# Performance work log

Hardware: AMD Instinct MI355X
Metric: run time of the kernel (lower is better)

The kernel has to match this reference:

```python
import jax, jax.numpy as jnp
import numpy as np

EPS = 1e-06
NUM_HEADS = 16


def _rms_norm(x, g, eps=EPS):
    # normalize over the last (full model) dim, as WanRMSNorm(dim)
    var = jnp.mean(jnp.square(x), axis=-1, keepdims=True)
    return x * jax.lax.rsqrt(var + eps) * g


def _apply_rope(q, k, freqs):
    # q, k: [b, s, n, d]; freqs: [s, d//2] angles. Interleaved (complex) pairs
    b, s, n, d = q.shape
    cos = jnp.cos(freqs)[None, :, None, :]  # [1, s, 1, d//2]
    sin = jnp.sin(freqs)[None, :, None, :]

    def rot(t):
        tr = t.reshape(b, s, n, d // 2, 2)
        t0, t1 = tr[..., 0], tr[..., 1]
        o0 = t0 * cos - t1 * sin
        o1 = t0 * sin + t1 * cos
        return jnp.stack([o0, o1], axis=-1).reshape(b, s, n, d)

    return rot(q), rot(k)


def setup_inputs() -> dict:
    key = jax.random.key(0)
    ks = jax.random.split(key, 8)
    b, s, dim = 2, 2048, 2048
    hd = dim // NUM_HEADS
    x = jax.random.normal(ks[0], (b, s, dim), dtype=jnp.float32)
    seq_lens = jax.random.randint(ks[1], (b,), s // 2, s + 1, dtype=jnp.int32)
    grid_sizes = jax.random.randint(ks[2], (b, 3), 1, 16).astype(jnp.int64)
    freqs = jax.random.uniform(ks[3], (s, hd // 2), dtype=jnp.float32) * 6.283
    sc = 1.0 / np.sqrt(dim)
    Wq = jax.random.normal(ks[4], (dim, dim), dtype=jnp.float32) * sc
    Wk = jax.random.normal(ks[5], (dim, dim), dtype=jnp.float32) * sc
    Wv = jax.random.normal(ks[6], (dim, dim), dtype=jnp.float32) * sc
    Wo = jax.random.normal(ks[7], (dim, dim), dtype=jnp.float32) * sc
    bo = jnp.zeros((dim,), dtype=jnp.float32)
    gq = jnp.ones((dim,), dtype=jnp.float32)
    gk = jnp.ones((dim,), dtype=jnp.float32)
    return {"x": x, "seq_lens": seq_lens, "grid_sizes": grid_sizes, "freqs": freqs,
            "Wq": Wq, "Wk": Wk, "Wv": Wv, "Wo": Wo, "bo": bo, "gq": gq, "gk": gk}


def reference(x, seq_lens, grid_sizes, freqs, Wq, Wk, Wv, Wo, bo, gq, gk):
    b, s, dim = x.shape
    n = NUM_HEADS
    d = dim // n
    scale = d ** (-0.5)

    # QKV projections (Linear: x @ W.T), with RMSNorm over full dim on q/k
    q = _rms_norm(x @ Wq.T, gq).reshape(b, s, n, d)
    k = _rms_norm(x @ Wk.T, gk).reshape(b, s, n, d)
    v = (x @ Wv.T).reshape(b, s, n, d)

    q, k = _apply_rope(q, k, freqs)

    # varlen attention: keys beyond seq_lens[b] are masked out
    scores = jnp.einsum("bqnd,bknd->bnqk", q, k) * scale
    key_valid = jnp.arange(s)[None, None, None, :] < seq_lens[:, None, None, None]
    scores = jnp.where(key_valid, scores, jnp.float32(-1e9))
    probs = jax.nn.softmax(scores, axis=-1)
    attn = jnp.einsum("bnqk,bknd->bqnd", probs, v).reshape(b, s, dim)

    return attn @ Wo.T + bo
```

## Files before the change

### kernel.cpp

```cpp
#include <hip/hip_runtime.h>
#include <hip/hip_bf16.h>
#include <math.h>

#define BATCH 2
#define SEQ   2048
#define DIM   2048
#define NH    16
#define HD    128
#define NROWS (BATCH * SEQ)
#define EPS_RMS 1e-6f

typedef unsigned short ushort_t;
typedef unsigned int   uint_t;
typedef __bf16    bf16x8 __attribute__((ext_vector_type(8)));
typedef _Float16  f16x8  __attribute__((ext_vector_type(8)));
typedef float     f32x4  __attribute__((ext_vector_type(4)));

__device__ inline ushort_t f2bf(float f) {
    uint_t u = __builtin_bit_cast(uint_t, f);
    uint_t r = u + 0x7FFFu + ((u >> 16) & 1u);
    return (ushort_t)(r >> 16);
}
__device__ inline ushort_t f2h(float f) {
    return __builtin_bit_cast(ushort_t, (_Float16)f);
}

__global__ __launch_bounds__(256) void cvt_all_kernel(
    const float* __restrict__ x,  const float* __restrict__ wq,
    const float* __restrict__ wk, const float* __restrict__ wv,
    const float* __restrict__ wo,
    ushort_t* __restrict__ xh,  ushort_t* __restrict__ wqh,
    ushort_t* __restrict__ wkh, ushort_t* __restrict__ wvh,
    ushort_t* __restrict__ woh)
{
    const int blk = blockIdx.x;
    const float* src; ushort_t* dst; size_t base;
    if (blk < 4096) { src = x; dst = xh; base = (size_t)blk * 2048; }
    else {
        const int r = blk - 4096;
        const int wsel = r >> 11;
        base = (size_t)(r & 2047) * 2048;
        if      (wsel == 0) { src = wq; dst = wqh; }
        else if (wsel == 1) { src = wk; dst = wkh; }
        else if (wsel == 2) { src = wv; dst = wvh; }
        else                { src = wo; dst = woh; }
    }
    const size_t i = base + ((size_t)threadIdx.x << 3);
    float v[8];
    *(float4*)&v[0] = *(const float4*)&src[i];
    *(float4*)&v[4] = *(const float4*)&src[i + 4];
    uint_t pk[4];
#pragma unroll
    for (int j = 0; j < 4; ++j)
        pk[j] = (uint_t)f2h(v[2 * j]) | ((uint_t)f2h(v[2 * j + 1]) << 16);
    *(uint4*)&dst[i] = make_uint4(pk[0], pk[1], pk[2], pk[3]);
}

template<int MODE>
__global__ __launch_bounds__(256, 3) void gemm_f16_kernel(
    const ushort_t* __restrict__ Ah, const ushort_t* __restrict__ Bh,
    const float* __restrict__ bias,
    float* __restrict__ C, ushort_t* __restrict__ Ct,
    const int M, const int N, const int K)
{
    __shared__ __align__(16) ushort_t sA[4096], sB[4096];
    const int tid  = threadIdx.x;
    const int w    = tid >> 6;
    const int lane = tid & 63;

    const int bid   = blockIdx.x;
    const int chunk = gridDim.x >> 3;
    const int nid   = (bid & 7) * chunk + (bid >> 3);
    const int mb    = M >> 7;
    const int n_blk = nid / mb;
    const int m_blk = nid - n_blk * mb;
    const int m0 = m_blk * 128;
    const int n0 = n_blk * 128;

    const int scol = (lane & 3) << 3;
    const int wr = w >> 1, wc = w & 1;
    const int fr = lane & 15, quad = lane >> 4;

    f32x4 acc[4][4];
#pragma unroll
    for (int mi = 0; mi < 4; ++mi)
#pragma unroll
        for (int ni = 0; ni < 4; ++ni)
            acc[mi][ni] = (f32x4){0.f, 0.f, 0.f, 0.f};

    for (int k0 = 0; k0 < K; k0 += 32) {
        __syncthreads();
#pragma unroll
        for (int it = 0; it < 2; ++it) {
            const int row  = (w << 5) + (it << 4) + (lane >> 2);
            const int loff = (w << 10) + (it << 9);
            const size_t ga = (size_t)(m0 + row) * K + k0 + scol;
            const size_t gb = (size_t)(n0 + row) * K + k0 + scol;
            __builtin_amdgcn_global_load_lds(
                (const __attribute__((address_space(1))) uint_t*)(const void*)(Ah + ga),
                (__attribute__((address_space(3))) uint_t*)(void*)&sA[loff], 16, 0, 0);
            __builtin_amdgcn_global_load_lds(
                (const __attribute__((address_space(1))) uint_t*)(const void*)(Bh + gb),
                (__attribute__((address_space(3))) uint_t*)(void*)&sB[loff], 16, 0, 0);
        }
        __syncthreads();

        f16x8 bfr[4];
#pragma unroll
        for (int ni = 0; ni < 4; ++ni) {
            const int row = (wc << 6) + (ni << 4) + fr;
            bfr[ni] = *(const f16x8*)&sB[(row << 5) + (quad << 3)];
        }
#pragma unroll
        for (int mi = 0; mi < 4; ++mi) {
            const int row = (wr << 6) + (mi << 4) + fr;
            const f16x8 ah = *(const f16x8*)&sA[(row << 5) + (quad << 3)];
#pragma unroll
            for (int ni = 0; ni < 4; ++ni)
                acc[mi][ni] = __builtin_amdgcn_mfma_f32_16x16x32_f16(ah, bfr[ni], acc[mi][ni], 0, 0, 0);
        }
    }

#pragma unroll
    for (int mi = 0; mi < 4; ++mi)
#pragma unroll
        for (int ni = 0; ni < 4; ++ni) {
            const int col = n0 + (wc << 6) + (ni << 4) + fr;
            if (MODE == 0) {
                const float bv = bias ? bias[col] : 0.f;
#pragma unroll
                for (int r = 0; r < 4; ++r) {
                    const int rowg = m0 + (wr << 6) + (mi << 4) + (quad << 2) + r;
                    C[(size_t)rowg * N + col] = acc[mi][ni][r] + bv;
                }
            } else {
                const int rowg = m0 + (wr << 6) + (mi << 4) + (quad << 2);
                const int bb = rowg >> 11, tok = rowg & (SEQ - 1);
                const int hh = col >> 7, d = col & (HD - 1);
                uint2 pk;
                pk.x = (uint_t)f2bf(acc[mi][ni][0]) | ((uint_t)f2bf(acc[mi][ni][1]) << 16);
                pk.y = (uint_t)f2bf(acc[mi][ni][2]) | ((uint_t)f2bf(acc[mi][ni][3]) << 16);
                *(uint2*)&Ct[((size_t)(bb * NH + hh) * HD + d) * SEQ + tok] = pk;
            }
        }
}

__global__ __launch_bounds__(256, 3) void qkv_gemm_kernel(
    const ushort_t* __restrict__ Ah, const ushort_t* __restrict__ Bq,
    const ushort_t* __restrict__ Bk, const ushort_t* __restrict__ Bv,
    float* __restrict__ Qb, float* __restrict__ Kb, ushort_t* __restrict__ Vt)
{
    __shared__ __align__(16) ushort_t sA[4096], sB[4096];
    const int tid  = threadIdx.x;
    const int w    = tid >> 6;
    const int lane = tid & 63;

    const int bid = blockIdx.x;
    const int nid = (bid & 7) * 192 + (bid >> 3);
    const int n_blk = nid >> 5;
    const int m_blk = nid & 31;
    const int wsel  = n_blk >> 4;
    const int m0 = m_blk * 128;
    const int n0 = (n_blk & 15) * 128;
    const ushort_t* __restrict__ Bh = (wsel == 0) ? Bq : (wsel == 1) ? Bk : Bv;

    const int scol = (lane & 3) << 3;
    const int wr = w >> 1, wc = w & 1;
    const int fr = lane & 15, quad = lane >> 4;

    f32x4 acc[4][4];
#pragma unroll
    for (int mi = 0; mi < 4; ++mi)
#pragma unroll
        for (int ni = 0; ni < 4; ++ni)
            acc[mi][ni] = (f32x4){0.f, 0.f, 0.f, 0.f};

    for (int k0 = 0; k0 < DIM; k0 += 32) {
        __syncthreads();
#pragma unroll
        for (int it = 0; it < 2; ++it) {
            const int row  = (w << 5) + (it << 4) + (lane >> 2);
            const int loff = (w << 10) + (it << 9);
            const size_t ga = (size_t)(m0 + row) * DIM + k0 + scol;
            const size_t gb = (size_t)(n0 + row) * DIM + k0 + scol;
            __builtin_amdgcn_global_load_lds(
                (const __attribute__((address_space(1))) uint_t*)(const void*)(Ah + ga),
                (__attribute__((address_space(3))) uint_t*)(void*)&sA[loff], 16, 0, 0);
            __builtin_amdgcn_global_load_lds(
                (const __attribute__((address_space(1))) uint_t*)(const void*)(Bh + gb),
                (__attribute__((address_space(3))) uint_t*)(void*)&sB[loff], 16, 0, 0);
        }
        __syncthreads();

        f16x8 bfr[4];
#pragma unroll
        for (int ni = 0; ni < 4; ++ni) {
            const int row = (wc << 6) + (ni << 4) + fr;
            bfr[ni] = *(const f16x8*)&sB[(row << 5) + (quad << 3)];
        }
#pragma unroll
        for (int mi = 0; mi < 4; ++mi) {
            const int row = (wr << 6) + (mi << 4) + fr;
            const f16x8 ah = *(const f16x8*)&sA[(row << 5) + (quad << 3)];
#pragma unroll
            for (int ni = 0; ni < 4; ++ni)
                acc[mi][ni] = __builtin_amdgcn_mfma_f32_16x16x32_f16(ah, bfr[ni], acc[mi][ni], 0, 0, 0);
        }
    }

    if (wsel < 2) {
        float* __restrict__ C = (wsel == 0) ? Qb : Kb;
#pragma unroll
        for (int mi = 0; mi < 4; ++mi)
#pragma unroll
            for (int ni = 0; ni < 4; ++ni) {
                const int col = n0 + (wc << 6) + (ni << 4) + fr;
#pragma unroll
                for (int r = 0; r < 4; ++r) {
                    const int rowg = m0 + (wr << 6) + (mi << 4) + (quad << 2) + r;
                    C[(size_t)rowg * DIM + col] = acc[mi][ni][r];
                }
            }
    } else {
#pragma unroll
        for (int mi = 0; mi < 4; ++mi)
#pragma unroll
            for (int ni = 0; ni < 4; ++ni) {
                const int col = n0 + (wc << 6) + (ni << 4) + fr;
                const int rowg = m0 + (wr << 6) + (mi << 4) + (quad << 2);
                const int bb = rowg >> 11, tok = rowg & (SEQ - 1);
                const int hh = col >> 7, d = col & (HD - 1);
                uint2 pk;
                pk.x = (uint_t)f2bf(acc[mi][ni][0]) | ((uint_t)f2bf(acc[mi][ni][1]) << 16);
                pk.y = (uint_t)f2bf(acc[mi][ni][2]) | ((uint_t)f2bf(acc[mi][ni][3]) << 16);
                *(uint2*)&Vt[((size_t)(bb * NH + hh) * HD + d) * SEQ + tok] = pk;
            }
    }
}

#define BM 64
#define BN 64
#define BK 16

__global__ __launch_bounds__(256) void gemm_nt_kernel(
    const float* __restrict__ A, const float* __restrict__ W,
    const float* __restrict__ bias, float* __restrict__ C,
    const int M, const int N, const int K)
{
    __shared__ float As[BK][BM + 4];
    __shared__ float Bs[BK][BN + 4];
    const int tid = threadIdx.x;
    const int tx = tid & 15;
    const int ty = tid >> 4;
    const int m0 = blockIdx.y * BM;
    const int n0 = blockIdx.x * BN;
    const int ldr = tid >> 2;
    const int ldc = (tid & 3) << 2;

    float acc[4][4] = {};

    for (int k0 = 0; k0 < K; k0 += BK) {
        __syncthreads();
        const float4 av = *(const float4*)&A[(size_t)(m0 + ldr) * K + (k0 + ldc)];
        const float4 wv = *(const float4*)&W[(size_t)(n0 + ldr) * K + (k0 + ldc)];
        As[ldc + 0][ldr] = av.x; As[ldc + 1][ldr] = av.y;
        As[ldc + 2][ldr] = av.z; As[ldc + 3][ldr] = av.w;
        Bs[ldc + 0][ldr] = wv.x; Bs[ldc + 1][ldr] = wv.y;
        Bs[ldc + 2][ldr] = wv.z; Bs[ldc + 3][ldr] = wv.w;
        __syncthreads();
#pragma unroll
        for (int k = 0; k < BK; ++k) {
            const float4 a4 = *(const float4*)&As[k][ty << 2];
            const float4 b4 = *(const float4*)&Bs[k][tx << 2];
            const float aa[4] = {a4.x, a4.y, a4.z, a4.w};
            const float bb[4] = {b4.x, b4.y, b4.z, b4.w};
#pragma unroll
            for (int i = 0; i < 4; ++i)
#pragma unroll
                for (int j = 0; j < 4; ++j)
                    acc[i][j] = fmaf(aa[i], bb[j], acc[i][j]);
        }
    }

#pragma unroll
    for (int i = 0; i < 4; ++i) {
        const int row = m0 + (ty << 2) + i;
        const int col = n0 + (tx << 2);
        float4 ov;
        ov.x = acc[i][0]; ov.y = acc[i][1]; ov.z = acc[i][2]; ov.w = acc[i][3];
        if (bias != nullptr) {
            ov.x += bias[col + 0]; ov.y += bias[col + 1];
            ov.z += bias[col + 2]; ov.w += bias[col + 3];
        }
        *(float4*)&C[(size_t)row * N + col] = ov;
    }
}

__global__ __launch_bounds__(256) void rmsnorm_rope_qk_kernel(
    const float* __restrict__ Qb, const float* __restrict__ gq,
    ushort_t* __restrict__ qbh,
    const float* __restrict__ Kb, const float* __restrict__ gk,
    ushort_t* __restrict__ kbh,
    const float* __restrict__ freqs)
{
    const int r = blockIdx.x;
    const int s = r & (SEQ - 1);
    const int tid = threadIdx.x;
    const int base = tid << 3;
    const bool isQ = (blockIdx.y == 0);
    const float* T = isQ ? Qb : Kb;
    const float* g = isQ ? gq : gk;
    ushort_t* out  = isQ ? qbh : kbh;
    const float posc = isQ ? 0.088388347648318447f : 1.0f;

    float v[8];
    *(float4*)&v[0] = *(const float4*)&T[(size_t)r * DIM + base];
    *(float4*)&v[4] = *(const float4*)&T[(size_t)r * DIM + base + 4];

    float ss = 0.f;
#pragma unroll
    for (int i = 0; i < 8; ++i) ss += v[i] * v[i];
#pragma unroll
    for (int off = 32; off > 0; off >>= 1) ss += __shfl_down(ss, off);

    __shared__ float wsum[4];
    __shared__ float inv_sh;
    if ((tid & 63) == 0) wsum[tid >> 6] = ss;
    __syncthreads();
    if (tid == 0)
        inv_sh = rsqrtf((wsum[0] + wsum[1] + wsum[2] + wsum[3]) * (1.0f / DIM) + EPS_RMS);
    __syncthreads();
    const float inv = inv_sh * posc;

    float gg[8];
    *(float4*)&gg[0] = *(const float4*)&g[base];
    *(float4*)&gg[4] = *(const float4*)&g[base + 4];
#pragma unroll
    for (int i = 0; i < 8; ++i) v[i] *= inv * gg[i];

    const int p0 = (base & (HD - 1)) >> 1;
#pragma unroll
    for (int pp = 0; pp < 4; ++pp) {
        float sn, cs;
        __sincosf(freqs[(size_t)s * (HD / 2) + p0 + pp], &sn, &cs);
        const float t0 = v[2 * pp], t1 = v[2 * pp + 1];
        v[2 * pp]     = t0 * cs - t1 * sn;
        v[2 * pp + 1] = t0 * sn + t1 * cs;
    }

    uint_t pk[4];
#pragma unroll
    for (int j = 0; j < 4; ++j)
        pk[j] = (uint_t)f2bf(v[2 * j]) | ((uint_t)f2bf(v[2 * j + 1]) << 16);
    *(uint4*)&out[(size_t)r * DIM + base] = make_uint4(pk[0], pk[1], pk[2], pk[3]);
}

__global__ __launch_bounds__(256) void rmsnorm_rope_kernel(
    float* __restrict__ T, const float* __restrict__ g,
    const float* __restrict__ freqs)
{
    const int r = blockIdx.x;
    const int s = r & (SEQ - 1);
    const int tid = threadIdx.x;
    const int base = tid << 3;

    float v[8];
    *(float4*)&v[0] = *(const float4*)&T[(size_t)r * DIM + base];
    *(float4*)&v[4] = *(const float4*)&T[(size_t)r * DIM + base + 4];

    float ss = 0.f;
#pragma unroll
    for (int i = 0; i < 8; ++i) ss += v[i] * v[i];
#pragma unroll
    for (int off = 32; off > 0; off >>= 1) ss += __shfl_down(ss, off);

    __shared__ float wsum[4];
    __shared__ float inv_sh;
    if ((tid & 63) == 0) wsum[tid >> 6] = ss;
    __syncthreads();
    if (tid == 0)
        inv_sh = rsqrtf((wsum[0] + wsum[1] + wsum[2] + wsum[3]) * (1.0f / DIM) + EPS_RMS);
    __syncthreads();
    const float inv = inv_sh;

    float gg[8];
    *(float4*)&gg[0] = *(const float4*)&g[base];
    *(float4*)&gg[4] = *(const float4*)&g[base + 4];
#pragma unroll
    for (int i = 0; i < 8; ++i) v[i] *= inv * gg[i];

    const int p0 = (base & (HD - 1)) >> 1;
#pragma unroll
    for (int pp = 0; pp < 4; ++pp) {
        float sn, cs;
        __sincosf(freqs[(size_t)s * (HD / 2) + p0 + pp], &sn, &cs);
        const float t0 = v[2 * pp], t1 = v[2 * pp + 1];
        v[2 * pp]     = t0 * cs - t1 * sn;
        v[2 * pp + 1] = t0 * sn + t1 * cs;
    }

    *(float4*)&T[(size_t)r * DIM + base]     = *(float4*)&v[0];
    *(float4*)&T[(size_t)r * DIM + base + 4] = *(float4*)&v[4];
}

#define AQ 128
#define AK 64
#define KSTR 136
#define VSTR 72
#define RESCALE_THR 8.0f

__global__ __launch_bounds__(256, 3) void attn_mfma_kernel(
    const ushort_t* __restrict__ QH, const ushort_t* __restrict__ KH,
    const ushort_t* __restrict__ VtG, const int* __restrict__ seq_lens,
    ushort_t* __restrict__ Oh)
{
    __shared__ __align__(16) ushort_t sK[AK * KSTR];
    __shared__ __align__(16) ushort_t sVt[HD * VSTR];
    __shared__ __align__(16) ushort_t sP[AQ * VSTR];

    const int tid  = threadIdx.x;
    const int w    = tid >> 6;
    const int lane = tid & 63;
    const int fr   = lane & 15;
    const int quad = lane >> 4;

    const int bid = blockIdx.x;
    const int sw  = (bid & 7) * 64 + (bid >> 3);
    const int q0  = (sw & 15) * AQ;
    const int hb  = sw >> 4;
    const int h   = hb & 15;
    const int b   = hb >> 4;
    const int len = seq_lens[b];

    bf16x8 qfrag[2][4];
#pragma unroll
    for (int qt = 0; qt < 2; ++qt)
#pragma unroll
        for (int h4 = 0; h4 < 4; ++h4) {
            const size_t qrow = (size_t)(b * SEQ + q0 + (w << 5) + (qt << 4) + fr);
            qfrag[qt][h4] = *(const bf16x8*)&QH[qrow * DIM + h * HD + (h4 << 5) + (quad << 3)];
        }

    f32x4 Oacc[2][8];
#pragma unroll
    for (int qt = 0; qt < 2; ++qt)
#pragma unroll
        for (int dt = 0; dt < 8; ++dt)
            Oacc[qt][dt] = (f32x4){0.f, 0.f, 0.f, 0.f};
    float mrow[2] = {-1.0e30f, -1.0e30f};
    float lrow[2] = {0.f, 0.f};

    const int kr  = tid >> 4;
    const int kc8 = (tid & 15) << 3;
    const int vd  = tid >> 3;
    const int vc8 = (tid & 7) << 3;
    const size_t kbase = (size_t)(b * SEQ) * DIM + h * HD + kc8;
    const size_t vbase = ((size_t)(b * NH + h) * HD) * SEQ + vc8;

    const int ntiles = (len + AK - 1) / AK;
    for (int t = 0; t < ntiles; ++t) {
        const int k0 = t * AK;
        const bool masked = (k0 + AK > len);
        __syncthreads();
        {
            uint4 kv[4], vv[4];
#pragma unroll
            for (int j = 0; j < 4; ++j)
                kv[j] = *(const uint4*)&KH[kbase + (size_t)(k0 + kr + (j << 4)) * DIM];
#pragma unroll
            for (int j = 0; j < 4; ++j)
                vv[j] = *(const uint4*)&VtG[vbase + (size_t)(vd + (j << 5)) * SEQ + k0];
#pragma unroll
            for (int j = 0; j < 4; ++j)
                *(uint4*)&sK[(kr + (j << 4)) * KSTR + kc8] = kv[j];
#pragma unroll
            for (int j = 0; j < 4; ++j)
                *(uint4*)&sVt[(vd + (j << 5)) * VSTR + vc8] = vv[j];
        }
        __syncthreads();

        f32x4 S[4][2];
        __builtin_amdgcn_s_setprio(1);
#pragma unroll
        for (int kt = 0; kt < 4; ++kt) {
            bf16x8 kf[4];
#pragma unroll
            for (int h4 = 0; h4 < 4; ++h4)
                kf[h4] = *(const bf16x8*)&sK[((kt << 4) + fr) * KSTR + (h4 << 5) + (quad << 3)];
#pragma unroll
            for (int qt = 0; qt < 2; ++qt) {
                f32x4 a = (f32x4){0.f, 0.f, 0.f, 0.f};
#pragma unroll
                for (int h4 = 0; h4 < 4; ++h4)
                    a = __builtin_amdgcn_mfma_f32_16x16x32_bf16(kf[h4], qfrag[qt][h4], a, 0, 0, 0);
                S[kt][qt] = a;
            }
        }
        __builtin_amdgcn_s_setprio(0);

#pragma unroll
        for (int qt = 0; qt < 2; ++qt) {
            float tm = -1.0e30f;
            if (masked) {
#pragma unroll
                for (int kt = 0; kt < 4; ++kt)
#pragma unroll
                    for (int r = 0; r < 4; ++r) {
                        const int key = k0 + (kt << 4) + (quad << 2) + r;
                        float s = (key < len) ? S[kt][qt][r] : -1.0e30f;
                        S[kt][qt][r] = s;
                        tm = fmaxf(tm, s);
                    }
            } else {
#pragma unroll
                for (int kt = 0; kt < 4; ++kt)
#pragma unroll
                    for (int r = 0; r < 4; ++r)
                        tm = fmaxf(tm, S[kt][qt][r]);
            }
            tm = fmaxf(tm, __shfl_xor(tm, 16));
            tm = fmaxf(tm, __shfl_xor(tm, 32));

            float mnew;
            if (__all(tm - mrow[qt] <= RESCALE_THR)) {
                mnew = mrow[qt];
            } else {
                mnew = fmaxf(mrow[qt], tm);
                const float alpha = __expf(mrow[qt] - mnew);
                mrow[qt] = mnew;
                lrow[qt] *= alpha;
#pragma unroll
                for (int r = 0; r < 4; ++r) {
                    const float ar = __shfl(alpha, (quad << 2) + r);
#pragma unroll
                    for (int dt = 0; dt < 8; ++dt)
                        Oacc[qt][dt][r] *= ar;
                }
            }

            float rsum = 0.f;
#pragma unroll
            for (int kt = 0; kt < 4; ++kt) {
                float p[4];
#pragma unroll
                for (int r = 0; r < 4; ++r) {
                    p[r] = __expf(S[kt][qt][r] - mnew);
                    rsum += p[r];
                }
                uint2 pk;
                pk.x = (uint_t)f2bf(p[0]) | ((uint_t)f2bf(p[1]) << 16);
                pk.y = (uint_t)f2bf(p[2]) | ((uint_t)f2bf(p[3]) << 16);
                *(uint2*)&sP[((w << 5) + (qt << 4) + fr) * VSTR + (kt << 4) + (quad << 2)] = pk;
            }
            rsum += __shfl_xor(rsum, 16);
            rsum += __shfl_xor(rsum, 32);
            lrow[qt] += rsum;
        }

        __builtin_amdgcn_s_setprio(1);
#pragma unroll
        for (int ks = 0; ks < 2; ++ks) {
            bf16x8 pf[2];
#pragma unroll
            for (int qt = 0; qt < 2; ++qt)
                pf[qt] = *(const bf16x8*)&sP[((w << 5) + (qt << 4) + fr) * VSTR + (ks << 5) + (quad << 3)];
#pragma unroll
            for (int dt = 0; dt < 8; ++dt) {
                const bf16x8 vf = *(const bf16x8*)&sVt[((dt << 4) + fr) * VSTR + (ks << 5) + (quad << 3)];
#pragma unroll
                for (int qt = 0; qt < 2; ++qt)
                    Oacc[qt][dt] = __builtin_amdgcn_mfma_f32_16x16x32_bf16(pf[qt], vf, Oacc[qt][dt], 0, 0, 0);
            }
        }
        __builtin_amdgcn_s_setprio(0);
    }

#pragma unroll
    for (int qt = 0; qt < 2; ++qt) {
        float linv[4];
#pragma unroll
        for (int r = 0; r < 4; ++r)
            linv[r] = 1.0f / __shfl(lrow[qt], (quad << 2) + r);
#pragma unroll
        for (int dt = 0; dt < 8; ++dt)
#pragma unroll
            for (int r = 0; r < 4; ++r) {
                const int qrow = q0 + (w << 5) + (qt << 4) + (quad << 2) + r;
                Oh[(size_t)(b * SEQ + qrow) * DIM + h * HD + (dt << 4) + fr] =
                    f2h(Oacc[qt][dt][r] * linv[r]);
            }
    }
}

#define BQ  64
#define BKT 64

__global__ __launch_bounds__(256) void attn_kernel(
    const float* __restrict__ Q, const float* __restrict__ K,
    const float* __restrict__ V, const int* __restrict__ seq_lens,
    float* __restrict__ O)
{
    const int qt = blockIdx.x;
    const int h  = blockIdx.y;
    const int b  = blockIdx.z;
    const int len = seq_lens[b];
    const int q0 = qt * BQ;
    const float scale = 0.088388347648318447f;

    __shared__ float Qst[HD][BQ + 4];
    __shared__ float Kst[HD][BKT + 4];
    __shared__ float Vs[BKT][HD + 4];
    __shared__ float Sc[BQ][BKT + 1];
    __shared__ float mrow[BQ], lrow[BQ], alpha_s[BQ];

    const int tid = threadIdx.x;
    const int si0 = (tid >> 4) << 2;
    const int sj0 = (tid & 15) << 2;
    const int pi0 = (tid >> 4) << 2;
    const int pc0 = (tid & 15) << 3;

    for (int i = tid; i < BQ * HD / 4; i += 256) {
        const int e = i << 2;
        const int row = e >> 7;
        const int c0 = e & (HD - 1);
        const float4 qv = *(const float4*)&Q[(size_t)(b * SEQ + q0 + row) * DIM + h * HD + c0];
        Qst[c0 + 0][row] = qv.x; Qst[c0 + 1][row] = qv.y;
        Qst[c0 + 2][row] = qv.z; Qst[c0 + 3][row] = qv.w;
    }
    if (tid < BQ) { mrow[tid] = -3.0e38f; lrow[tid] = 0.f; }

    float o[4][8] = {};
    __syncthreads();

    const int ntiles = (len + BKT - 1) / BKT;
    for (int t = 0; t < ntiles; ++t) {
        const int k0 = t * BKT;
        __syncthreads();
        for (int i = tid; i < BKT * HD / 4; i += 256) {
            const int e = i << 2;
            const int row = e >> 7;
            const int c0 = e & (HD - 1);
            const int kg = k0 + row;
            float4 kv = make_float4(0.f, 0.f, 0.f, 0.f);
            float4 vv = make_float4(0.f, 0.f, 0.f, 0.f);
            if (kg < len) {
                kv = *(const float4*)&K[(size_t)(b * SEQ + kg) * DIM + h * HD + c0];
                vv = *(const float4*)&V[(size_t)(b * SEQ + kg) * DIM + h * HD + c0];
            }
            Kst[c0 + 0][row] = kv.x; Kst[c0 + 1][row] = kv.y;
            Kst[c0 + 2][row] = kv.z; Kst[c0 + 3][row] = kv.w;
            *(float4*)&Vs[row][c0] = vv;
        }
        __syncthreads();

        float acc[4][4] = {};
#pragma unroll 8
        for (int kk = 0; kk < HD; ++kk) {
            const float4 q4 = *(const float4*)&Qst[kk][si0];
            const float4 k4 = *(const float4*)&Kst[kk][sj0];
            const float qa[4] = {q4.x, q4.y, q4.z, q4.w};
            const float ka[4] = {k4.x, k4.y, k4.z, k4.w};
#pragma unroll
            for (int i = 0; i < 4; ++i)
#pragma unroll
                for (int j = 0; j < 4; ++j)
                    acc[i][j] = fmaf(qa[i], ka[j], acc[i][j]);
        }
#pragma unroll
        for (int i = 0; i < 4; ++i)
#pragma unroll
            for (int j = 0; j < 4; ++j) {
                const int jg = k0 + sj0 + j;
                Sc[si0 + i][sj0 + j] = (jg < len) ? acc[i][j] * scale : -1.0e9f;
            }
        __syncthreads();

        if (tid < BQ) {
            const int i = tid;
            const float m_old = mrow[i];
            float mx = m_old;
            for (int j = 0; j < BKT; ++j) mx = fmaxf(mx, Sc[i][j]);
            const float al = __expf(m_old - mx);
            float sum = 0.f;
            for (int j = 0; j < BKT; ++j) {
                const float p = __expf(Sc[i][j] - mx);
                Sc[i][j] = p;
                sum += p;
            }
            mrow[i] = mx;
            lrow[i] = lrow[i] * al + sum;
            alpha_s[i] = al;
        }
        __syncthreads();

#pragma unroll
        for (int i = 0; i < 4; ++i) {
            const float al = alpha_s[pi0 + i];
#pragma unroll
            for (int c = 0; c < 8; ++c) o[i][c] *= al;
        }
        for (int j = 0; j < BKT; ++j) {
            float p[4];
#pragma unroll
            for (int i = 0; i < 4; ++i) p[i] = Sc[pi0 + i][j];
            const float4 v0 = *(const float4*)&Vs[j][pc0];
            const float4 v1 = *(const float4*)&Vs[j][pc0 + 4];
            const float va[8] = {v0.x, v0.y, v0.z, v0.w, v1.x, v1.y, v1.z, v1.w};
#pragma unroll
            for (int i = 0; i < 4; ++i)
#pragma unroll
                for (int c = 0; c < 8; ++c)
                    o[i][c] = fmaf(p[i], va[c], o[i][c]);
        }
    }

#pragma unroll
    for (int i = 0; i < 4; ++i) {
        const float invl = 1.0f / lrow[pi0 + i];
        float4 w0, w1;
        w0.x = o[i][0] * invl; w0.y = o[i][1] * invl;
        w0.z = o[i][2] * invl; w0.w = o[i][3] * invl;
        w1.x = o[i][4] * invl; w1.y = o[i][5] * invl;
        w1.z = o[i][6] * invl; w1.w = o[i][7] * invl;
        float* op = &O[(size_t)(b * SEQ + q0 + pi0 + i) * DIM + h * HD + pc0];
        *(float4*)&op[0] = w0;
        *(float4*)&op[4] = w1;
    }
}

extern "C" void kernel_launch(void* const* d_in, const int* in_sizes, int n_in,
                              void* d_out, int out_size, void* d_ws, size_t ws_size,
                              hipStream_t stream)
{
    const float* x        = (const float*)d_in[0];
    const int*   seq_lens = (const int*)d_in[1];
    const float* freqs    = (const float*)d_in[3];
    const float* Wq       = (const float*)d_in[4];
    const float* Wk       = (const float*)d_in[5];
    const float* Wv       = (const float*)d_in[6];
    const float* Wo       = (const float*)d_in[7];
    const float* bo       = (const float*)d_in[8];
    const float* gq       = (const float*)d_in[9];
    const float* gk       = (const float*)d_in[10];
    float* out = (float*)d_out;

    const size_t mat = (size_t)NROWS * DIM;
    const size_t wsz = (size_t)DIM * DIM;

    float*    Qb   = (float*)d_ws;
    float*    Kb   = Qb + mat;
    ushort_t* xh   = (ushort_t*)(Kb + mat);
    ushort_t* wqh  = xh + mat;
    ushort_t* wkh  = wqh + wsz;
    ushort_t* wvh  = wkh + wsz;
    ushort_t* woh  = wvh + wsz;
    ushort_t* qbh  = woh + wsz;
    ushort_t* kbh  = qbh + mat;
    ushort_t* vtg  = kbh + mat;
    ushort_t* abh  = vtg + mat;

    const size_t need = 2 * mat * sizeof(float)
                      + (mat + 4 * wsz + 4 * mat) * sizeof(ushort_t);

    if (ws_size >= need) {
        cvt_all_kernel<<<12288, 256, 0, stream>>>(
            x, Wq, Wk, Wv, Wo, xh, wqh, wkh, wvh, woh);

        qkv_gemm_kernel<<<1536, 256, 0, stream>>>(xh, wqh, wkh, wvh, Qb, Kb, vtg);

        rmsnorm_rope_qk_kernel<<<dim3(NROWS, 2), 256, 0, stream>>>(
            Qb, gq, qbh, Kb, gk, kbh, freqs);

        attn_mfma_kernel<<<512, 256, 0, stream>>>(qbh, kbh, vtg, seq_lens, abh);

        gemm_f16_kernel<0><<<512, 256, 0, stream>>>(abh, woh, bo, out, nullptr, NROWS, DIM, DIM);
    } else {
        float* Vb = Kb + mat;
        float* Ab = Vb + mat;
        const dim3 gemm_grid(DIM / BN, NROWS / BM);
        gemm_nt_kernel<<<gemm_grid, 256, 0, stream>>>(x, Wq, nullptr, Qb, NROWS, DIM, DIM);
        gemm_nt_kernel<<<gemm_grid, 256, 0, stream>>>(x, Wk, nullptr, Kb, NROWS, DIM, DIM);
        gemm_nt_kernel<<<gemm_grid, 256, 0, stream>>>(x, Wv, nullptr, Vb, NROWS, DIM, DIM);
        rmsnorm_rope_kernel<<<NROWS, 256, 0, stream>>>(Qb, gq, freqs);
        rmsnorm_rope_kernel<<<NROWS, 256, 0, stream>>>(Kb, gk, freqs);
        attn_kernel<<<dim3(SEQ / BQ, NH, BATCH), 256, 0, stream>>>(Qb, Kb, Vb, seq_lens, Ab);
        gemm_nt_kernel<<<gemm_grid, 256, 0, stream>>>(Ab, Wo, bo, out, NROWS, DIM, DIM);
    }
}
```

Measured before the change: 452.0 us.

## Rewrite QKV GEMM with 256x256 tiles, double-buffered async LDS loads and swizzle

The QKV projection GEMM moves from 128x128 tiles with BK=32 and single buffering to 256x256 tiles, 512 threads, BK=64 and two LDS buffers. Global-to-LDS loads for tile k+2 are interleaved between MFMA phases using explicit vmcnt waits, sched barriers and s_setprio. An XOR swizzle is applied to the LDS layout to avoid bank conflicts. The aim is more reuse per loaded byte and hiding memory latency behind compute. In exchange, LDS use grows to 128 KB per block and register pressure rises, which limits occupancy, and the grid shrinks to 384 blocks.

```diff
diff --git a/kernel.cpp b/kernel.cpp
--- a/kernel.cpp
+++ b/kernel.cpp
@@ -145,95 +145,149 @@
         }
 }
 
-__global__ __launch_bounds__(256, 3) void qkv_gemm_kernel(
+__global__ __launch_bounds__(512, 2) void qkv_gemm_kernel(
     const ushort_t* __restrict__ Ah, const ushort_t* __restrict__ Bq,
     const ushort_t* __restrict__ Bk, const ushort_t* __restrict__ Bv,
     float* __restrict__ Qb, float* __restrict__ Kb, ushort_t* __restrict__ Vt)
 {
-    __shared__ __align__(16) ushort_t sA[4096], sB[4096];
+    __shared__ __align__(16) ushort_t sA[32768];
+    __shared__ __align__(16) ushort_t sB[32768];
     const int tid  = threadIdx.x;
     const int w    = tid >> 6;
     const int lane = tid & 63;
-
-    const int bid = blockIdx.x;
-    const int nid = (bid & 7) * 192 + (bid >> 3);
-    const int n_blk = nid >> 5;
-    const int m_blk = nid & 31;
-    const int wsel  = n_blk >> 4;
-    const int m0 = m_blk * 128;
-    const int n0 = (n_blk & 15) * 128;
+    const int fr   = lane & 15;
+    const int quad = lane >> 4;
+    const int wr   = w >> 2;
+    const int wc   = w & 3;
+
+    const int bid   = blockIdx.x;
+    const int nid   = (bid & 7) * 48 + (bid >> 3);
+    const int n_blk = nid >> 4;
+    const int m_blk = nid & 15;
+    const int wsel  = n_blk >> 3;
+    const int m0    = m_blk << 8;
+    const int n0    = (n_blk & 7) << 8;
     const ushort_t* __restrict__ Bh = (wsel == 0) ? Bq : (wsel == 1) ? Bk : Bv;
 
-    const int scol = (lane & 3) << 3;
-    const int wr = w >> 1, wc = w & 1;
-    const int fr = lane & 15, quad = lane >> 4;
-
-    f32x4 acc[4][4];
-#pragma unroll
-    for (int mi = 0; mi < 4; ++mi)
+    const int rt  = tid >> 3;
+    const int csw = ((tid & 7) ^ (rt & 7)) << 3;
+    const size_t abg = (size_t)(m0 + rt) * DIM + csw;
+    const size_t bbg = (size_t)(n0 + rt) * DIM + csw;
+    const int lw  = w << 9;
+    const int axor = (fr & 7) << 4;
+
+#define QG(dst, src) __builtin_amdgcn_global_load_lds( \
+        (const __attribute__((address_space(1))) uint_t*)(const void*)(src), \
+        (__attribute__((address_space(3))) uint_t*)(void*)(dst), 16, 0, 0)
+#define QSA(buf, kt, q) QG(sA + ((buf) << 14) + ((q) << 12) + lw, \
+                           Ah + abg + ((size_t)(q) << 17) + ((size_t)(kt) << 6))
+#define QSB(buf, kt, q) QG(sB + ((buf) << 14) + ((q) << 12) + lw, \
+                           Bh + bbg + ((size_t)(q) << 17) + ((size_t)(kt) << 6))
+
+    f32x4 acc[8][4];
+#pragma unroll
+    for (int mi = 0; mi < 8; ++mi)
 #pragma unroll
         for (int ni = 0; ni < 4; ++ni)
             acc[mi][ni] = (f32x4){0.f, 0.f, 0.f, 0.f};
 
-    for (int k0 = 0; k0 < DIM; k0 += 32) {
-        __syncthreads();
-#pragma unroll
-        for (int it = 0; it < 2; ++it) {
-            const int row  = (w << 5) + (it << 4) + (lane >> 2);
-            const int loff = (w << 10) + (it << 9);
-            const size_t ga = (size_t)(m0 + row) * DIM + k0 + scol;
-            const size_t gb = (size_t)(n0 + row) * DIM + k0 + scol;
-            __builtin_amdgcn_global_load_lds(
-                (const __attribute__((address_space(1))) uint_t*)(const void*)(Ah + ga),
-                (__attribute__((address_space(3))) uint_t*)(void*)&sA[loff], 16, 0, 0);
-            __builtin_amdgcn_global_load_lds(
-                (const __attribute__((address_space(1))) uint_t*)(const void*)(Bh + gb),
-                (__attribute__((address_space(3))) uint_t*)(void*)&sB[loff], 16, 0, 0);
-        }
-        __syncthreads();
-
-        f16x8 bfr[4];
+#pragma unroll
+    for (int q = 0; q < 4; ++q) { QSA(0, 0, q); QSB(0, 0, q); }
+#pragma unroll
+    for (int q = 0; q < 4; ++q) { QSA(1, 1, q); QSB(1, 1, q); }
+    asm volatile("s_waitcnt vmcnt(8)" ::: "memory");
+    __builtin_amdgcn_sched_barrier(0);
+    __builtin_amdgcn_s_barrier();
+    __builtin_amdgcn_sched_barrier(0);
+
+#define QPHASE(MB)                                                              \
+        {                                                                       \
+            f16x8 af[2][2];                                                     \
+            _Pragma("unroll")                                                   \
+            for (int m2 = 0; m2 < 2; ++m2)                                      \
+                _Pragma("unroll")                                               \
+                for (int ks = 0; ks < 2; ++ks)                                  \
+                    af[m2][ks] = *(const f16x8*)(sAc +                          \
+                        (((wr << 7) + (((MB) + m2) << 4) + fr) << 7) +          \
+                        (((ks << 6) + (quad << 4)) ^ axor));                    \
+            __builtin_amdgcn_s_setprio(1);                                      \
+            _Pragma("unroll")                                                   \
+            for (int ks = 0; ks < 2; ++ks)                                      \
+                _Pragma("unroll")                                               \
+                for (int m2 = 0; m2 < 2; ++m2)                                  \
+                    _Pragma("unroll")                                           \
+                    for (int ni = 0; ni < 4; ++ni)                              \
+                        acc[(MB) + m2][ni] = __builtin_amdgcn_mfma_f32_16x16x32_f16( \
+                            af[m2][ks], bfr[ni][ks], acc[(MB) + m2][ni], 0, 0, 0); \
+            __builtin_amdgcn_s_setprio(0);                                      \
+        }                                                                       \
+        __builtin_amdgcn_sched_barrier(0);                                      \
+        __builtin_amdgcn_s_barrier();                                           \
+        __builtin_amdgcn_sched_barrier(0);
+
+    for (int kt = 0; kt < 32; ++kt) {
+        const int cur = kt & 1;
+        const char* sAc = (const char*)sA + (cur << 15);
+        const char* sBc = (const char*)sB + (cur << 15);
+        const bool pf = (kt < 30);
+
+        f16x8 bfr[4][2];
 #pragma unroll
         for (int ni = 0; ni < 4; ++ni) {
-            const int row = (wc << 6) + (ni << 4) + fr;
-            bfr[ni] = *(const f16x8*)&sB[(row << 5) + (quad << 3)];
-        }
-#pragma unroll
-        for (int mi = 0; mi < 4; ++mi) {
-            const int row = (wr << 6) + (mi << 4) + fr;
-            const f16x8 ah = *(const f16x8*)&sA[(row << 5) + (quad << 3)];
-#pragma unroll
-            for (int ni = 0; ni < 4; ++ni)
-                acc[mi][ni] = __builtin_amdgcn_mfma_f32_16x16x32_f16(ah, bfr[ni], acc[mi][ni], 0, 0, 0);
-        }
-    }
+            const int brow = (wc << 6) + (ni << 4) + fr;
+#pragma unroll
+            for (int ks = 0; ks < 2; ++ks)
+                bfr[ni][ks] = *(const f16x8*)(sBc + brow * 128 +
+                    (((ks << 6) + (quad << 4)) ^ ((brow & 7) << 4)));
+        }
+        QPHASE(0)
+        if (pf) { QSB(cur, kt + 2, 0); QSB(cur, kt + 2, 1);
+                  QSB(cur, kt + 2, 2); QSB(cur, kt + 2, 3); }
+        QPHASE(2)
+        if (pf) { QSA(cur, kt + 2, 0); QSA(cur, kt + 2, 2); }
+        QPHASE(4)
+        QPHASE(6)
+        if (pf) {
+            QSA(cur, kt + 2, 1); QSA(cur, kt + 2, 3);
+            asm volatile("s_waitcnt vmcnt(8)" ::: "memory");
+        } else {
+            asm volatile("s_waitcnt vmcnt(0)" ::: "memory");
+        }
+        __builtin_amdgcn_sched_barrier(0);
+        __builtin_amdgcn_s_barrier();
+        __builtin_amdgcn_sched_barrier(0);
+    }
+#undef QPHASE
+#undef QSA
+#undef QSB
+#undef QG
 
     if (wsel < 2) {
         float* __restrict__ C = (wsel == 0) ? Qb : Kb;
 #pragma unroll
-        for (int mi = 0; mi < 4; ++mi)
+        for (int mi = 0; mi < 8; ++mi)
 #pragma unroll
             for (int ni = 0; ni < 4; ++ni) {
                 const int col = n0 + (wc << 6) + (ni << 4) + fr;
 #pragma unroll
                 for (int r = 0; r < 4; ++r) {
-                    const int rowg = m0 + (wr << 6) + (mi << 4) + (quad << 2) + r;
+                    const int rowg = m0 + (wr << 7) + (mi << 4) + (quad << 2) + r;
                     C[(size_t)rowg * DIM + col] = acc[mi][ni][r];
                 }
             }
     } else {
 #pragma unroll
-        for (int mi = 0; mi < 4; ++mi)
+        for (int mi = 0; mi < 8; ++mi)
 #pragma unroll
             for (int ni = 0; ni < 4; ++ni) {
                 const int col = n0 + (wc << 6) + (ni << 4) + fr;
-                const int rowg = m0 + (wr << 6) + (mi << 4) + (quad << 2);
-                const int bb = rowg >> 11, tok = rowg & (SEQ - 1);
+                const int rowg = m0 + (wr << 7) + (mi << 4) + (quad << 2);
+                const int bbi = rowg >> 11, tok = rowg & (SEQ - 1);
                 const int hh = col >> 7, d = col & (HD - 1);
                 uint2 pk;
                 pk.x = (uint_t)f2bf(acc[mi][ni][0]) | ((uint_t)f2bf(acc[mi][ni][1]) << 16);
                 pk.y = (uint_t)f2bf(acc[mi][ni][2]) | ((uint_t)f2bf(acc[mi][ni][3]) << 16);
-                *(uint2*)&Vt[((size_t)(bb * NH + hh) * HD + d) * SEQ + tok] = pk;
+                *(uint2*)&Vt[((size_t)(bbi * NH + hh) * HD + d) * SEQ + tok] = pk;
             }
     }
 }
@@ -766,7 +820,7 @@
         cvt_all_kernel<<<12288, 256, 0, stream>>>(
             x, Wq, Wk, Wv, Wo, xh, wqh, wkh, wvh, woh);
 
-        qkv_gemm_kernel<<<1536, 256, 0, stream>>>(xh, wqh, wkh, wvh, Qb, Kb, vtg);
+        qkv_gemm_kernel<<<384, 512, 0, stream>>>(xh, wqh, wkh, wvh, Qb, Kb, vtg);
 
         rmsnorm_rope_qk_kernel<<<dim3(NROWS, 2), 256, 0, stream>>>(
             Qb, gq, qbh, Kb, gk, kbh, freqs);
```

Measured after the change: 452.8 us. About the same (+0.2%).
